# Optimization experiments

Measured on AMD Instinct MI355X. Metric: run time of the kernel, lower is better.

## Reference

```python
import jax, jax.numpy as jnp
import numpy as np

B, S, D, FF, H, N, P, K, KP, R = 2, 512, 256, 1024, 4, 512, 32, 16, 4, 64
DH = D // H  # 64


def _ln(x, g, b):
    mu = x.mean(-1, keepdims=True)
    var = ((x - mu) ** 2).mean(-1, keepdims=True)
    return (x - mu) * jax.lax.rsqrt(var + 1e-5) * g + b


def setup_inputs() -> dict:
    key = jax.random.key(0)
    ks = iter(jax.random.split(key, 40))
    nrm = lambda shape, std=0.02: jax.random.normal(next(ks), shape, jnp.float32) * std
    return dict(
        x=jax.random.normal(next(ks), (B, S, D), jnp.float32),
        g1=jnp.ones((D,), jnp.float32), b1=jnp.zeros((D,), jnp.float32),
        g2=jnp.ones((D,), jnp.float32), b2=jnp.zeros((D,), jnp.float32),
        Wq=nrm((D, D)), bq=jnp.zeros((D,), jnp.float32),
        Wk=nrm((D, D)), bk=jnp.zeros((D,), jnp.float32),
        Wv=nrm((D, D)), bv=jnp.zeros((D,), jnp.float32),
        Wpath=nrm((2 * D, 2)), bpath=jnp.zeros((2,), jnp.float32),
        neurons=nrm((N, D)),
        Wnq=nrm((D, D)), bnq=jnp.zeros((D,), jnp.float32),
        Wnk=nrm((D, D)), bnk=jnp.zeros((D,), jnp.float32),
        Wnv=nrm((D, D)), bnv=jnp.zeros((D,), jnp.float32),
        pattern_queries=nrm((P, D)),
        pattern_up_A=nrm((P, D, R)),
        pattern_up_B=nrm((P, R, FF), 0.01),
        Wub=nrm((D, FF), 0.01), bub=jnp.zeros((FF,), jnp.float32),
        Wd=nrm((FF, D), 0.02), bd=jnp.zeros((D,), jnp.float32),
    )


def _forward(x, g1, b1, g2, b2, Wq, bq, Wk, bk, Wv, bv, Wpath, bpath, neurons,
             Wnq, bnq, Wnk, bnk, Wnv, bnv, pattern_queries, pattern_up_A,
             pattern_up_B, Wub, bub, Wd, bd):
    # ---- NeuronRouter on norm1(x) ----
    n1 = _ln(x, g1, b1)
    q = (n1 @ Wq + bq).reshape(B, S, H, DH)
    k = (n1 @ Wk + bk).reshape(B, S, H, DH)
    v = (n1 @ Wv + bv).reshape(B, S, H, DH)
    attn = jax.nn.softmax(jnp.einsum('bqhd,bkhd->bhqk', q, k) / np.float32(np.sqrt(DH)), axis=-1)
    context = jnp.einsum('bhqk,bkhd->bqhd', attn, v).reshape(B, S, D)
    token_scores = n1 @ neurons.T        # [B,S,N]
    context_scores = context @ neurons.T
    w = jax.nn.softmax(jnp.concatenate([n1, context], -1) @ Wpath + bpath, axis=-1)
    scores = w[..., 0:1] * token_scores + w[..., 1:2] * context_scores
    topk_scores, topk_idx = jax.lax.top_k(scores, K)
    topk_w = jax.nn.softmax(topk_scores, axis=-1)      # [B,S,K]
    selected = neurons[topk_idx]                        # [B,S,K,D]

    # ---- InteractionFFN on norm2(x) ----
    n2 = _ln(x, g2, b2)
    qn = (selected @ Wnq + bnq).reshape(B, S, K, H, DH)
    kn = (selected @ Wnk + bnk).reshape(B, S, K, H, DH)
    vn = jax.nn.sigmoid((selected @ Wnv + bnv).reshape(B, S, K, H, DH))
    aw = jax.nn.softmax(jnp.einsum('bsqhd,bskhd->bshqk', qn, kn) / np.float32(np.sqrt(DH)), axis=-1)
    gates = jnp.einsum('bshqk,bskhd->bsqhd', aw, vn).reshape(B, S, K, D)
    aggregated = jnp.sum(topk_w[..., None] * (selected * gates), axis=2)  # [B,S,D]

    pattern_scores = 0.5 * (aggregated @ pattern_queries.T) / np.float32(np.sqrt(D)) \
                     + 0.5 * (context @ pattern_queries.T)               # [B,S,P]
    tps, tpi = jax.lax.top_k(pattern_scores, KP)
    tpw = jax.nn.softmax(tps, axis=-1)                                   # [B,S,KP]

    combined = n2 + aggregated
    A = pattern_up_A[tpi]    # [B,S,KP,D,R]  (gathered per-token LoRA A)
    Bm = pattern_up_B[tpi]   # [B,S,KP,R,FF] (gathered per-token LoRA B)
    h_mid = jnp.einsum('bsd,bskdr->bskr', combined, A)
    h_pat = jnp.einsum('bskr,bskrf->bskf', h_mid, Bm)
    h_pattern = jnp.sum(tpw[..., None] * h_pat, axis=2)                  # [B,S,FF]
    h = jax.nn.gelu(0.1 * (combined @ Wub + bub) + 0.9 * h_pattern, approximate=False)
    out = h @ Wd + bd
    return x + out, topk_idx


def reference(x, g1, b1, g2, b2, Wq, bq, Wk, bk, Wv, bv, Wpath, bpath, neurons,
              Wnq, bnq, Wnk, bnk, Wnv, bnv, pattern_queries, pattern_up_A,
              pattern_up_B, Wub, bub, Wd, bd):
    return _forward(x, g1, b1, g2, b2, Wq, bq, Wk, bk, Wv, bv, Wpath, bpath,
                    neurons, Wnq, bnq, Wnk, bnk, Wnv, bnv, pattern_queries,
                    pattern_up_A, pattern_up_B, Wub, bub, Wd, bd)
```

## Files before the change

kernel.cpp:

```cpp
#include <hip/hip_runtime.h>
#include <hip/hip_bf16.h>
#include <math.h>

#define BB 2
#define SS 512
#define DD 256
#define FFD 1024
#define HH 4
#define NN 512
#define PP 32
#define KK 16
#define KPP 4
#define RR 64
#define DHH 64
#define TT (BB*SS)
#define QT 16

__global__ __launch_bounds__(64) void zero_kernel(int* __restrict__ p, int n)
{
    int i = threadIdx.x;
    if (i < n) p[i] = 0;
}

__global__ __launch_bounds__(256) void ln_kernel(
    const float* __restrict__ x,
    const float* __restrict__ g1, const float* __restrict__ b1,
    const float* __restrict__ g2, const float* __restrict__ b2,
    float* __restrict__ n1, float* __restrict__ n2)
{
    int t = blockIdx.x;
    int d = threadIdx.x;
    __shared__ float red[256];
    float v = x[t*DD + d];
    red[d] = v; __syncthreads();
    for (int s = 128; s > 0; s >>= 1) { if (d < s) red[d] += red[d+s]; __syncthreads(); }
    float mu = red[0] * (1.0f/DD);
    __syncthreads();
    float dv = v - mu;
    red[d] = dv*dv; __syncthreads();
    for (int s = 128; s > 0; s >>= 1) { if (d < s) red[d] += red[d+s]; __syncthreads(); }
    float var = red[0] * (1.0f/DD);
    float r = 1.0f / sqrtf(var + 1e-5f);
    n1[t*DD+d] = dv*r*g1[d] + b1[d];
    n2[t*DD+d] = dv*r*g2[d] + b2[d];
}

__device__ __forceinline__ void gemm_body(
    const float* __restrict__ A, const float* __restrict__ Bm,
    const float* __restrict__ bias, const float* __restrict__ extra,
    float* __restrict__ C, int M, int Nn, int Kk, int transB, int mode,
    int k0off, int kLen)
{
    __shared__ float As[2][32][68];
    __shared__ float Bs[2][32][68];
    int bm = blockIdx.y * 64;
    int bn = blockIdx.x * 64;
    int tid = threadIdx.x;
    int tx = tid & 15, ty = tid >> 4;

    float4 pa[2], pb[2];

    #define LOAD_A(kbase) { \
        _Pragma("unroll") \
        for (int e = 0; e < 2; ++e) { \
            int r = e*32 + (tid>>3); int c4 = tid & 7; \
            pa[e] = *(const float4*)&A[(size_t)(bm + r)*Kk + (kbase) + c4*4]; \
        } }
    #define STORE_A(buf) { \
        _Pragma("unroll") \
        for (int e = 0; e < 2; ++e) { \
            int r = e*32 + (tid>>3); int c4 = tid & 7; \
            As[buf][c4*4+0][r] = pa[e].x; \
            As[buf][c4*4+1][r] = pa[e].y; \
            As[buf][c4*4+2][r] = pa[e].z; \
            As[buf][c4*4+3][r] = pa[e].w; \
        } }
    #define LOAD_B(kbase) { \
        if (transB == 0) { \
            _Pragma("unroll") \
            for (int e = 0; e < 2; ++e) { \
                int c = e*16 + (tid>>4); int n4 = tid & 15; \
                pb[e] = *(const float4*)&Bm[(size_t)((kbase) + c)*Nn + bn + n4*4]; \
            } \
        } else { \
            _Pragma("unroll") \
            for (int e = 0; e < 2; ++e) { \
                int r = e*32 + (tid>>3); int k4 = tid & 7; \
                pb[e] = *(const float4*)&Bm[(size_t)(bn + r)*Kk + (kbase) + k4*4]; \
            } \
        } }
    #define STORE_B(buf) { \
        if (transB == 0) { \
            _Pragma("unroll") \
            for (int e = 0; e < 2; ++e) { \
                int c = e*16 + (tid>>4); int n4 = tid & 15; \
                *(float4*)&Bs[buf][c][n4*4] = pb[e]; \
            } \
        } else { \
            _Pragma("unroll") \
            for (int e = 0; e < 2; ++e) { \
                int r = e*32 + (tid>>3); int k4 = tid & 7; \
                Bs[buf][k4*4+0][r] = pb[e].x; \
                Bs[buf][k4*4+1][r] = pb[e].y; \
                Bs[buf][k4*4+2][r] = pb[e].z; \
                Bs[buf][k4*4+3][r] = pb[e].w; \
            } \
        } }

    float acc[4][4] = {};
    int nk = kLen >> 5;

    LOAD_A(k0off); LOAD_B(k0off);
    STORE_A(0); STORE_B(0);
    __syncthreads();

    for (int kt = 0; kt < nk; ++kt) {
        int cur = kt & 1;
        if (kt + 1 < nk) { LOAD_A(k0off + (kt+1)*32); LOAD_B(k0off + (kt+1)*32); }
        #pragma unroll
        for (int kk = 0; kk < 32; ++kk) {
            float4 av = *(const float4*)&As[cur][kk][ty*4];
            float4 bv = *(const float4*)&Bs[cur][kk][tx*4];
            acc[0][0] = fmaf(av.x, bv.x, acc[0][0]);
            acc[0][1] = fmaf(av.x, bv.y, acc[0][1]);
            acc[0][2] = fmaf(av.x, bv.z, acc[0][2]);
            acc[0][3] = fmaf(av.x, bv.w, acc[0][3]);
            acc[1][0] = fmaf(av.y, bv.x, acc[1][0]);
            acc[1][1] = fmaf(av.y, bv.y, acc[1][1]);
            acc[1][2] = fmaf(av.y, bv.z, acc[1][2]);
            acc[1][3] = fmaf(av.y, bv.w, acc[1][3]);
            acc[2][0] = fmaf(av.z, bv.x, acc[2][0]);
            acc[2][1] = fmaf(av.z, bv.y, acc[2][1]);
            acc[2][2] = fmaf(av.z, bv.z, acc[2][2]);
            acc[2][3] = fmaf(av.z, bv.w, acc[2][3]);
            acc[3][0] = fmaf(av.w, bv.x, acc[3][0]);
            acc[3][1] = fmaf(av.w, bv.y, acc[3][1]);
            acc[3][2] = fmaf(av.w, bv.z, acc[3][2]);
            acc[3][3] = fmaf(av.w, bv.w, acc[3][3]);
        }
        if (kt + 1 < nk) {
            STORE_A(cur^1); STORE_B(cur^1);
            __syncthreads();
        }
    }

    #pragma unroll
    for (int i = 0; i < 4; ++i) {
        int m = bm + ty*4 + i;
        #pragma unroll
        for (int j = 0; j < 4; ++j) {
            int n = bn + tx*4 + j;
            float val = acc[i][j] + (bias ? bias[n] : 0.0f);
            if (mode == 1) {
                val = 1.0f / (1.0f + expf(-val));
            } else if (mode == 2) {
                size_t idx = (size_t)m*Nn + n;
                float hp = extra[idx] + extra[idx + (size_t)TT*FFD]
                         + extra[idx + 2*(size_t)TT*FFD] + extra[idx + 3*(size_t)TT*FFD];
                float z = 0.1f*val + 0.9f*hp;
                val = 0.5f*z*(1.0f + erff(z*0.70710678118654752f));
            } else if (mode == 3) {
                val = val + extra[(size_t)m*Nn+n];
            }
            C[(size_t)m*Nn + n] = val;
        }
    }
    #undef LOAD_A
    #undef STORE_A
    #undef LOAD_B
    #undef STORE_B
}

__global__ __launch_bounds__(256) void gemm_kernel(
    const float* __restrict__ A, const float* __restrict__ Bm,
    const float* __restrict__ bias, const float* __restrict__ extra,
    float* __restrict__ C, int M, int Nn, int Kk, int transB, int mode)
{
    gemm_body(A, Bm, bias, extra, C, M, Nn, Kk, transB, mode, 0, Kk);
}

struct GemmSet { const float* A; const float* B; const float* bias; float* C; int mode; };

__global__ __launch_bounds__(256) void gemm3_kernel(
    GemmSet s0, GemmSet s1, GemmSet s2, int M, int Nn, int Kk, int transB)
{
    GemmSet s = (blockIdx.z == 0) ? s0 : ((blockIdx.z == 1) ? s1 : s2);
    gemm_body(s.A, s.B, s.bias, nullptr, s.C, M, Nn, Kk, transB, s.mode, 0, Kk);
}

__global__ __launch_bounds__(256) void gemm_splitk_kernel(
    const float* __restrict__ A, const float* __restrict__ Bm,
    float* __restrict__ Cpart, int M, int Nn, int Kk, int kPerSplit)
{
    int sk = blockIdx.z;
    float* Cp = Cpart + (size_t)sk * M * Nn;
    gemm_body(A, Bm, nullptr, nullptr, Cp, M, Nn, Kk, 0, 0, sk*kPerSplit, kPerSplit);
}

__global__ __launch_bounds__(256) void combine_wd_kernel(
    const float* __restrict__ part, const float* __restrict__ x,
    const float* __restrict__ bd, float* __restrict__ out)
{
    int i = blockIdx.x*256 + threadIdx.x;
    int d = i & (DD-1);
    float s = x[i] + bd[d];
    s += part[i] + part[i + TT*DD] + part[i + 2*TT*DD] + part[i + 3*TT*DD];
    out[i] = s;
}

__global__ __launch_bounds__(256) void attn_kernel(
    const float* __restrict__ q, const float* __restrict__ k,
    const float* __restrict__ v, float* __restrict__ ctx)
{
    int bi = blockIdx.x;
    int qt = bi & 31;
    int bh = bi >> 5;
    int h = bh & (HH-1);
    int b = bh >> 2;
    int tid = threadIdx.x;
    int qo = tid >> 4;
    int c  = tid & 15;

    __shared__ float Qs[QT][68];
    __shared__ float Kt[64][64];
    __shared__ float Vs[64][68];
    __shared__ float Ps[QT][68];

    {
        const float* qp = q + ((size_t)(b*SS + qt*QT + qo)*DD) + h*DHH + c*4;
        *(float4*)&Qs[qo][c*4] = *(const float4*)qp;
    }
    float O0=0.f, O1=0.f, O2=0.f, O3=0.f;
    float mreg = -3.4e38f, lreg = 0.f;

    for (int t = 0; t < 8; ++t) {
        if (t) __syncthreads();
        #pragma unroll
        for (int e = 0; e < 4; ++e) {
            int lin = e*256 + tid;
            int kr = lin & 63;
            int c4 = lin >> 6;
            const float* kp = k + ((size_t)(b*SS + t*64 + kr)*DD) + h*DHH + c4*4;
            float4 kv = *(const float4*)kp;
            Kt[c4*4+0][kr] = kv.x;
            Kt[c4*4+1][kr] = kv.y;
            Kt[c4*4+2][kr] = kv.z;
            Kt[c4*4+3][kr] = kv.w;
            int vr = lin >> 4;
            int vc = lin & 15;
            const float* vp = v + ((size_t)(b*SS + t*64 + vr)*DD) + h*DHH + vc*4;
            *(float4*)&Vs[vr][vc*4] = *(const float4*)vp;
        }
        __syncthreads();
        float s0=0.f, s1=0.f, s2=0.f, s3=0.f;
        #pragma unroll 8
        for (int d = 0; d < 64; ++d) {
            float qv = Qs[qo][d];
            float4 kv = *(const float4*)&Kt[d][c*4];
            s0 = fmaf(qv, kv.x, s0);
            s1 = fmaf(qv, kv.y, s1);
            s2 = fmaf(qv, kv.z, s2);
            s3 = fmaf(qv, kv.w, s3);
        }
        s0 *= 0.125f; s1 *= 0.125f; s2 *= 0.125f; s3 *= 0.125f;
        float mx = fmaxf(fmaxf(s0, s1), fmaxf(s2, s3));
        #pragma unroll
        for (int mk = 1; mk <= 8; mk <<= 1)
            mx = fmaxf(mx, __shfl_xor(mx, mk));
        float mnew = fmaxf(mreg, mx);
        float scl = __expf(mreg - mnew);
        float e0 = __expf(s0 - mnew), e1 = __expf(s1 - mnew),
              e2 = __expf(s2 - mnew), e3 = __expf(s3 - mnew);
        float esum = e0 + e1 + e2 + e3;
        #pragma unroll
        for (int mk = 1; mk <= 8; mk <<= 1)
            esum += __shfl_xor(esum, mk);
        lreg = lreg * scl + esum;
        mreg = mnew;
        float4 pw; pw.x = e0; pw.y = e1; pw.z = e2; pw.w = e3;
        *(float4*)&Ps[qo][c*4] = pw;
        __syncthreads();
        O0 *= scl; O1 *= scl; O2 *= scl; O3 *= scl;
        #pragma unroll 8
        for (int kk = 0; kk < 64; ++kk) {
            float pv = Ps[qo][kk];
            float4 vv = *(const float4*)&Vs[kk][c*4];
            O0 = fmaf(pv, vv.x, O0);
            O1 = fmaf(pv, vv.y, O1);
            O2 = fmaf(pv, vv.z, O2);
            O3 = fmaf(pv, vv.w, O3);
        }
    }
    float linv = 1.0f / lreg;
    float4 o4; o4.x = O0*linv; o4.y = O1*linv; o4.z = O2*linv; o4.w = O3*linv;
    *(float4*)(ctx + ((size_t)(b*SS + qt*QT + qo)*DD) + h*DHH + c*4) = o4;
}

__global__ __launch_bounds__(256) void route_kernel(
    const float* __restrict__ n1, const float* __restrict__ ctx,
    const float* __restrict__ Wpath, const float* __restrict__ bpath,
    const float* __restrict__ ts, const float* __restrict__ cs,
    int* __restrict__ topk_idx, float* __restrict__ topk_w,
    float* __restrict__ out_idx)
{
    int t = blockIdx.x, tid = threadIdx.x;
    int wv = tid >> 6;
    __shared__ float pw0[4], pw1[4];
    float a = n1[t*DD+tid], c = ctx[t*DD+tid];
    float r0 = a * Wpath[tid*2+0] + c * Wpath[(DD+tid)*2+0];
    float r1 = a * Wpath[tid*2+1] + c * Wpath[(DD+tid)*2+1];
    #pragma unroll
    for (int off = 1; off < 64; off <<= 1) {
        r0 += __shfl_xor(r0, off);
        r1 += __shfl_xor(r1, off);
    }
    if ((tid & 63) == 0) { pw0[wv] = r0; pw1[wv] = r1; }
    __syncthreads();
    __shared__ float w0s, w1s;
    if (tid == 0) {
        float l0 = pw0[0]+pw0[1]+pw0[2]+pw0[3] + bpath[0];
        float l1 = pw1[0]+pw1[1]+pw1[2]+pw1[3] + bpath[1];
        float mm = fmaxf(l0, l1);
        float e0 = expf(l0-mm), e1 = expf(l1-mm);
        float is = 1.0f/(e0+e1);
        w0s = e0*is; w1s = e1*is;
    }
    __syncthreads();
    float w0 = w0s, w1 = w1s;
    __shared__ float sc[NN];
    sc[tid]     = w0*ts[t*NN+tid]     + w1*cs[t*NN+tid];
    sc[tid+256] = w0*ts[t*NN+tid+256] + w1*cs[t*NN+tid+256];
    __syncthreads();
    __shared__ float wvv[4]; __shared__ int wvi[4];
    __shared__ float selv[KK]; __shared__ int seli[KK];
    for (int it = 0; it < KK; ++it) {
        float v0 = sc[tid], v1 = sc[tid+256];
        float bv; int bi;
        if (v0 >= v1) { bv = v0; bi = tid; } else { bv = v1; bi = tid+256; }
        #pragma unroll
        for (int off = 1; off < 64; off <<= 1) {
            float ov = __shfl_xor(bv, off);
            int   oi = __shfl_xor(bi, off);
            if (ov > bv || (ov == bv && oi < bi)) { bv = ov; bi = oi; }
        }
        if ((tid & 63) == 0) { wvv[wv] = bv; wvi[wv] = bi; }
        __syncthreads();
        if (tid == 0) {
            float fv = wvv[0]; int fi = wvi[0];
            #pragma unroll
            for (int w = 1; w < 4; ++w) {
                float ov = wvv[w]; int oi = wvi[w];
                if (ov > fv || (ov == fv && oi < fi)) { fv = ov; fi = oi; }
            }
            selv[it] = fv; seli[it] = fi; sc[fi] = -3.4e38f;
        }
        __syncthreads();
    }
    if (tid == 0) {
        float mx = selv[0];
        float e[KK]; float sum = 0.f;
        for (int i = 0; i < KK; ++i) { e[i] = expf(selv[i]-mx); sum += e[i]; }
        float is = 1.0f/sum;
        for (int i = 0; i < KK; ++i) {
            topk_idx[t*KK+i] = seli[i];
            topk_w[t*KK+i]   = e[i]*is;
            out_idx[t*KK+i]  = (float)seli[i];
        }
    }
}

__global__ __launch_bounds__(256) void interact_kernel(
    const float* __restrict__ neurons,
    const float* __restrict__ nqa, const float* __restrict__ nka,
    const float* __restrict__ nva,
    const int* __restrict__ topk_idx, const float* __restrict__ topk_w,
    float* __restrict__ agg)
{
    int t = blockIdx.x, tid = threadIdx.x;
    __shared__ float nq[KK][DD+1];
    __shared__ float nk[KK][DD+1];
    __shared__ float nv[KK][DD+1];
    __shared__ float ps[HH][KK][KK];
    __shared__ float tw[KK];
    __shared__ int sidx[KK];
    if (tid < KK) { tw[tid] = topk_w[t*KK+tid]; sidx[tid] = topk_idx[t*KK+tid]; }
    __syncthreads();
    for (int i = 0; i < KK; ++i) {
        int idx = sidx[i];
        nq[i][tid] = nqa[idx*DD+tid];
        nk[i][tid] = nka[idx*DD+tid];
        nv[i][tid] = nva[idx*DD+tid];
    }
    __syncthreads();
    #pragma unroll
    for (int r = 0; r < 4; ++r) {
        int lin = r*256 + tid;
        int j = lin & 15, i = (lin >> 4) & 15, h = lin >> 8;
        const float* qp = &nq[i][h*DHH];
        const float* kp = &nk[j][h*DHH];
        float acc = 0.f;
        #pragma unroll 8
        for (int d = 0; d < DHH; ++d) acc = fmaf(qp[d], kp[d], acc);
        ps[h][i][j] = acc * 0.125f;
    }
    __syncthreads();
    if (tid < 64) {
        int h = tid >> 4, i = tid & 15;
        float mx = -3.4e38f;
        for (int j = 0; j < KK; ++j) mx = fmaxf(mx, ps[h][i][j]);
        float sum = 0.f;
        for (int j = 0; j < KK; ++j) { float e = expf(ps[h][i][j]-mx); ps[h][i][j] = e; sum += e; }
        float is = 1.0f/sum;
        for (int j = 0; j < KK; ++j) ps[h][i][j] *= is;
    }
    __syncthreads();
    int d = tid, h = d >> 6;
    float acc = 0.f;
    for (int i = 0; i < KK; ++i) {
        float g = 0.f;
        #pragma unroll
        for (int j = 0; j < KK; ++j) g = fmaf(ps[h][i][j], nv[j][d], g);
        acc += tw[i] * neurons[sidx[i]*DD + d] * g;
    }
    agg[t*DD+d] = acc;
}

__global__ __launch_bounds__(256) void pattern_select(
    const float* __restrict__ aggp, const float* __restrict__ ctxp,
    const float* __restrict__ n2p, const float* __restrict__ PQ,
    float* __restrict__ combined, float* __restrict__ tpwg,
    int* __restrict__ bin_count, int* __restrict__ bin_entry)
{
    int t = blockIdx.x, tid = threadIdx.x;
    __shared__ float mix[DD];
    __shared__ float ps[PP];
    __shared__ float psp[8][33];
    __shared__ int tpi[KPP];

    float a = aggp[t*DD+tid];
    float cx = ctxp[t*DD+tid];
    mix[tid] = 0.03125f * a + 0.5f * cx;
    combined[t*DD+tid] = n2p[t*DD+tid] + a;
    __syncthreads();

    {
        int p = tid & 31, g = tid >> 5;
        const float* pq = PQ + p*DD + g*32;
        const float* mp = mix + g*32;
        float acc = 0.f;
        #pragma unroll
        for (int d = 0; d < 32; ++d) acc = fmaf(mp[d], pq[d], acc);
        psp[g][p] = acc;
    }
    __syncthreads();
    if (tid < PP) {
        float s = 0.f;
        #pragma unroll
        for (int g = 0; g < 8; ++g) s += psp[g][tid];
        ps[tid] = s;
    }
    __syncthreads();

    if (tid == 0) {
        float vals[KPP];
        #pragma unroll
        for (int it = 0; it < KPP; ++it) {
            float bv = -3.4e38f; int bi = 0;
            for (int p = 0; p < PP; ++p) { float v = ps[p]; if (v > bv) { bv = v; bi = p; } }
            vals[it] = bv; tpi[it] = bi; ps[bi] = -3.4e38f;
        }
        float mx = vals[0];
        float e0 = expf(vals[0]-mx), e1 = expf(vals[1]-mx),
              e2 = expf(vals[2]-mx), e3 = expf(vals[3]-mx);
        float is = 1.0f/(e0+e1+e2+e3);
        tpwg[t*4+0]=e0*is; tpwg[t*4+1]=e1*is; tpwg[t*4+2]=e2*is; tpwg[t*4+3]=e3*is;
    }
    __syncthreads();
    if (tid < KPP) {
        int p = tpi[tid];
        int slot = atomicAdd(&bin_count[p], 1);
        bin_entry[p*TT + slot] = (t << 2) | tid;
    }
}

__global__ __launch_bounds__(256) void pattern_apply(
    const float* __restrict__ comb, const float* __restrict__ tpwg,
    const int* __restrict__ bin_count, const int* __restrict__ bin_entry,
    const float* __restrict__ Aup, const float* __restrict__ Bup,
    float* __restrict__ hpat4)
{
    int p = blockIdx.y, cch = blockIdx.x;
    int cnt = bin_count[p];
    int base = cch * 16;
    if (base >= cnt) return;
    int nt = cnt - base; if (nt > 16) nt = 16;
    int tid = threadIdx.x;

    __shared__ int toks[16]; __shared__ int kps[16]; __shared__ float wts[16];
    __shared__ float combs[16][DD+1];
    __shared__ float hmid[16][RR];

    if (tid < 16) {
        if (tid < nt) {
            int e = bin_entry[p*TT + base + tid];
            int t = e >> 2, kp = e & 3;
            toks[tid] = t; kps[tid] = kp; wts[tid] = tpwg[t*4 + kp];
        } else { toks[tid] = -1; wts[tid] = 0.f; }
    }
    __syncthreads();
    #pragma unroll
    for (int i = 0; i < 16; ++i) {
        int t = toks[i];
        combs[i][tid] = (t >= 0) ? comb[(size_t)t*DD + tid] : 0.f;
    }
    __syncthreads();

    {
        int i = tid >> 4, g = tid & 15;
        const float* Ap = Aup + (size_t)p*(DD*RR) + g*4;
        float a0=0.f, a1=0.f, a2=0.f, a3=0.f;
        #pragma unroll 8
        for (int d = 0; d < DD; ++d) {
            float cv = combs[i][d];
            float4 av = *(const float4*)&Ap[(size_t)d*RR];
            a0 = fmaf(cv, av.x, a0);
            a1 = fmaf(cv, av.y, a1);
            a2 = fmaf(cv, av.z, a2);
            a3 = fmaf(cv, av.w, a3);
        }
        float w = wts[i];
        hmid[i][g*4+0] = a0*w;
        hmid[i][g*4+1] = a1*w;
        hmid[i][g*4+2] = a2*w;
        hmid[i][g*4+3] = a3*w;
    }
    __syncthreads();

    float4 acc[16];
    #pragma unroll
    for (int i = 0; i < 16; ++i) acc[i] = make_float4(0.f,0.f,0.f,0.f);
    const float* Bp = Bup + (size_t)p*(RR*FFD) + tid*4;
    for (int r4 = 0; r4 < RR/4; ++r4) {
        float4 b0 = *(const float4*)&Bp[(size_t)(r4*4+0)*FFD];
        float4 b1 = *(const float4*)&Bp[(size_t)(r4*4+1)*FFD];
        float4 b2 = *(const float4*)&Bp[(size_t)(r4*4+2)*FFD];
        float4 b3 = *(const float4*)&Bp[(size_t)(r4*4+3)*FFD];
        #pragma unroll
        for (int i = 0; i < 16; ++i) {
            float4 h = *(const float4*)&hmid[i][r4*4];
            acc[i].x = fmaf(h.x,b0.x, fmaf(h.y,b1.x, fmaf(h.z,b2.x, fmaf(h.w,b3.x, acc[i].x))));
            acc[i].y = fmaf(h.x,b0.y, fmaf(h.y,b1.y, fmaf(h.z,b2.y, fmaf(h.w,b3.y, acc[i].y))));
            acc[i].z = fmaf(h.x,b0.z, fmaf(h.y,b1.z, fmaf(h.z,b2.z, fmaf(h.w,b3.z, acc[i].z))));
            acc[i].w = fmaf(h.x,b0.w, fmaf(h.y,b1.w, fmaf(h.z,b2.w, fmaf(h.w,b3.w, acc[i].w))));
        }
    }
    #pragma unroll
    for (int i = 0; i < 16; ++i) {
        int t = toks[i];
        if (t >= 0)
            *(float4*)&hpat4[(size_t)kps[i]*(TT*FFD) + (size_t)t*FFD + tid*4] = acc[i];
    }
}

extern "C" void kernel_launch(void* const* d_in, const int* in_sizes, int n_in,
                              void* d_out, int out_size, void* d_ws, size_t ws_size,
                              hipStream_t stream)
{
    const float* x        = (const float*)d_in[0];
    const float* g1       = (const float*)d_in[1];
    const float* b1       = (const float*)d_in[2];
    const float* g2       = (const float*)d_in[3];
    const float* b2       = (const float*)d_in[4];
    const float* Wq       = (const float*)d_in[5];
    const float* bq       = (const float*)d_in[6];
    const float* Wk       = (const float*)d_in[7];
    const float* bk       = (const float*)d_in[8];
    const float* Wv       = (const float*)d_in[9];
    const float* bv       = (const float*)d_in[10];
    const float* Wpath    = (const float*)d_in[11];
    const float* bpath    = (const float*)d_in[12];
    const float* neurons  = (const float*)d_in[13];
    const float* Wnq      = (const float*)d_in[14];
    const float* bnq      = (const float*)d_in[15];
    const float* Wnk      = (const float*)d_in[16];
    const float* bnk      = (const float*)d_in[17];
    const float* Wnv      = (const float*)d_in[18];
    const float* bnv      = (const float*)d_in[19];
    const float* PQ       = (const float*)d_in[20];
    const float* Aup      = (const float*)d_in[21];
    const float* Bup      = (const float*)d_in[22];
    const float* Wub      = (const float*)d_in[23];
    const float* bub      = (const float*)d_in[24];
    const float* Wd       = (const float*)d_in[25];
    const float* bd       = (const float*)d_in[26];

    float* out0    = (float*)d_out;
    float* out_idx = out0 + (size_t)TT*DD;

    float* ws = (float*)d_ws;
    float* n1    = ws; ws += TT*DD;
    float* n2    = ws; ws += TT*DD;
    float* qb    = ws; ws += TT*DD;
    float* kb    = ws; ws += TT*DD;
    float* vb    = ws; ws += TT*DD;
    float* ctx   = ws; ws += TT*DD;
    float* ts    = ws; ws += TT*NN;
    float* cs    = ws; ws += TT*NN;
    float* nqa   = ws; ws += NN*DD;
    float* nka   = ws; ws += NN*DD;
    float* nva   = ws; ws += NN*DD;
    float* agg   = ws; ws += TT*DD;
    float* comb  = ws; ws += TT*DD;
    float* hpat4 = ws; ws += 4*TT*FFD;
    float* hb    = ws; ws += TT*FFD;
    float* part  = ws; ws += 4*TT*DD;
    float* tkw   = ws; ws += TT*KK;
    float* tpwg  = ws; ws += TT*KPP;
    int*   tki   = (int*)ws; ws += TT*KK;
    int*   binc  = (int*)ws; ws += 32;
    int*   bine  = (int*)ws; ws += 32*TT;

    dim3 blk(256);

    zero_kernel<<<1, 64, 0, stream>>>(binc, 32);

    ln_kernel<<<TT, blk, 0, stream>>>(x, g1, b1, g2, b2, n1, n2);

    {
        GemmSet sq{n1, Wq, bq, qb, 0}, sk{n1, Wk, bk, kb, 0}, sv{n1, Wv, bv, vb, 0};
        gemm3_kernel<<<dim3(DD/64, TT/64, 3), blk, 0, stream>>>(sq, sk, sv, TT, DD, DD, 0);
    }

    {
        GemmSet s0{neurons, Wnq, bnq, nqa, 0}, s1{neurons, Wnk, bnk, nka, 0},
                s2{neurons, Wnv, bnv, nva, 1};
        gemm3_kernel<<<dim3(DD/64, NN/64, 3), blk, 0, stream>>>(s0, s1, s2, NN, DD, DD, 0);
    }

    attn_kernel<<<BB*HH*(SS/QT), blk, 0, stream>>>(qb, kb, vb, ctx);

    {
        GemmSet s0{n1, neurons, nullptr, ts, 0}, s1{ctx, neurons, nullptr, cs, 0};
        gemm3_kernel<<<dim3(NN/64, TT/64, 2), blk, 0, stream>>>(s0, s1, s1, TT, NN, DD, 1);
    }

    route_kernel<<<TT, blk, 0, stream>>>(n1, ctx, Wpath, bpath, ts, cs, tki, tkw, out_idx);

    interact_kernel<<<TT, blk, 0, stream>>>(neurons, nqa, nka, nva, tki, tkw, agg);

    pattern_select<<<TT, blk, 0, stream>>>(agg, ctx, n2, PQ, comb, tpwg, binc, bine);

    pattern_apply<<<dim3(TT/16, PP), blk, 0, stream>>>(comb, tpwg, binc, bine, Aup, Bup, hpat4);

    gemm_kernel<<<dim3(FFD/64, TT/64), blk, 0, stream>>>(comb, Wub, bub, hpat4, hb, TT, FFD, DD, 0, 2);

    gemm_splitk_kernel<<<dim3(DD/64, TT/64, 4), blk, 0, stream>>>(hb, Wd, part, TT, DD, FFD, FFD/4);
    combine_wd_kernel<<<TT*DD/256, blk, 0, stream>>>(part, x, bd, out0);
}
```

Baseline: 342.3 us.

## Split pattern LoRA into two kernels staging A and B tiles in LDS

The fused per-16-token pattern_apply kernel is split into two kernels. lora_mid loads each pattern's A matrix (64 KB) into shared memory once and loops over that pattern's bin entries, writing the weighted mid activations to a new global buffer. lora_apply tiles the FF dimension into 128-wide slices, keeps the B slice in LDS and processes entries in chunks of 64. The goal is to stop re-reading A and B from global memory for every 16-token chunk. The cost is an extra launch, a round trip through global memory for the mid activations, and a large LDS footprint that lowers occupancy, while load imbalance across uneven bins may serialise some blocks.

```diff
diff --git a/kernel.cpp b/kernel.cpp
--- a/kernel.cpp
+++ b/kernel.cpp
@@ -483,82 +483,122 @@
     }
 }
 
-__global__ __launch_bounds__(256) void pattern_apply(
+__global__ __launch_bounds__(256) void lora_mid(
     const float* __restrict__ comb, const float* __restrict__ tpwg,
     const int* __restrict__ bin_count, const int* __restrict__ bin_entry,
-    const float* __restrict__ Aup, const float* __restrict__ Bup,
-    float* __restrict__ hpat4)
-{
-    int p = blockIdx.y, cch = blockIdx.x;
+    const float* __restrict__ Aup, float* __restrict__ hmid_g)
+{
+    int p = blockIdx.x, sub = blockIdx.y;
     int cnt = bin_count[p];
-    int base = cch * 16;
-    if (base >= cnt) return;
-    int nt = cnt - base; if (nt > 16) nt = 16;
+    if (sub * 16 >= cnt) return;
     int tid = threadIdx.x;
 
-    __shared__ int toks[16]; __shared__ int kps[16]; __shared__ float wts[16];
-    __shared__ float combs[16][DD+1];
-    __shared__ float hmid[16][RR];
-
-    if (tid < 16) {
-        if (tid < nt) {
-            int e = bin_entry[p*TT + base + tid];
-            int t = e >> 2, kp = e & 3;
-            toks[tid] = t; kps[tid] = kp; wts[tid] = tpwg[t*4 + kp];
-        } else { toks[tid] = -1; wts[tid] = 0.f; }
-    }
-    __syncthreads();
+    __shared__ float As[DD][RR];
+    __shared__ float combs[16][DD+4];
+    __shared__ int es[16];
+
+    const float* Ap = Aup + (size_t)p*(DD*RR);
     #pragma unroll
-    for (int i = 0; i < 16; ++i) {
-        int t = toks[i];
-        combs[i][tid] = (t >= 0) ? comb[(size_t)t*DD + tid] : 0.f;
-    }
-    __syncthreads();
-
-    {
-        int i = tid >> 4, g = tid & 15;
-        const float* Ap = Aup + (size_t)p*(DD*RR) + g*4;
+    for (int e = 0; e < 64; ++e) {
+        int lin = e*256 + tid;
+        int d = lin >> 4, rg = lin & 15;
+        *(float4*)&As[d][rg*4] = *(const float4*)&Ap[(size_t)d*RR + rg*4];
+    }
+
+    for (int base = sub*16; base < cnt; base += 8*16) {
+        int nt = cnt - base; if (nt > 16) nt = 16;
+        __syncthreads();
+        if (tid < 16) es[tid] = (tid < nt) ? bin_entry[p*TT + base + tid] : -1;
+        __syncthreads();
+        #pragma unroll
+        for (int i = 0; i < 16; ++i) {
+            int e = es[i];
+            combs[i][tid] = (e >= 0) ? comb[(size_t)(e >> 2)*DD + tid] : 0.f;
+        }
+        __syncthreads();
+
+        int i = tid >> 4, rg = tid & 15;
         float a0=0.f, a1=0.f, a2=0.f, a3=0.f;
         #pragma unroll 8
         for (int d = 0; d < DD; ++d) {
             float cv = combs[i][d];
-            float4 av = *(const float4*)&Ap[(size_t)d*RR];
+            float4 av = *(const float4*)&As[d][rg*4];
             a0 = fmaf(cv, av.x, a0);
             a1 = fmaf(cv, av.y, a1);
             a2 = fmaf(cv, av.z, a2);
             a3 = fmaf(cv, av.w, a3);
         }
-        float w = wts[i];
-        hmid[i][g*4+0] = a0*w;
-        hmid[i][g*4+1] = a1*w;
-        hmid[i][g*4+2] = a2*w;
-        hmid[i][g*4+3] = a3*w;
-    }
-    __syncthreads();
-
-    float4 acc[16];
+        int e = es[i];
+        if (e >= 0) {
+            float w = tpwg[e];
+            float4 o; o.x = a0*w; o.y = a1*w; o.z = a2*w; o.w = a3*w;
+            *(float4*)&hmid_g[(size_t)e*RR + rg*4] = o;
+        }
+    }
+}
+
+__global__ __launch_bounds__(256) void lora_apply(
+    const int* __restrict__ bin_count, const int* __restrict__ bin_entry,
+    const float* __restrict__ hmid_g, const float* __restrict__ Bup,
+    float* __restrict__ hpat4)
+{
+    int p = blockIdx.x, ff0 = blockIdx.y * 128;
+    int cnt = bin_count[p];
+    int tid = threadIdx.x;
+
+    __shared__ float Bs[RR][132];
+    __shared__ float hm[64][68];
+    __shared__ int es[64];
+
+    const float* Bp = Bup + (size_t)p*(RR*FFD) + ff0;
     #pragma unroll
-    for (int i = 0; i < 16; ++i) acc[i] = make_float4(0.f,0.f,0.f,0.f);
-    const float* Bp = Bup + (size_t)p*(RR*FFD) + tid*4;
-    for (int r4 = 0; r4 < RR/4; ++r4) {
-        float4 b0 = *(const float4*)&Bp[(size_t)(r4*4+0)*FFD];
-        float4 b1 = *(const float4*)&Bp[(size_t)(r4*4+1)*FFD];
-        float4 b2 = *(const float4*)&Bp[(size_t)(r4*4+2)*FFD];
-        float4 b3 = *(const float4*)&Bp[(size_t)(r4*4+3)*FFD];
-        #pragma unroll
-        for (int i = 0; i < 16; ++i) {
-            float4 h = *(const float4*)&hmid[i][r4*4];
-            acc[i].x = fmaf(h.x,b0.x, fmaf(h.y,b1.x, fmaf(h.z,b2.x, fmaf(h.w,b3.x, acc[i].x))));
-            acc[i].y = fmaf(h.x,b0.y, fmaf(h.y,b1.y, fmaf(h.z,b2.y, fmaf(h.w,b3.y, acc[i].y))));
-            acc[i].z = fmaf(h.x,b0.z, fmaf(h.y,b1.z, fmaf(h.z,b2.z, fmaf(h.w,b3.z, acc[i].z))));
-            acc[i].w = fmaf(h.x,b0.w, fmaf(h.y,b1.w, fmaf(h.z,b2.w, fmaf(h.w,b3.w, acc[i].w))));
-        }
-    }
-    #pragma unroll
-    for (int i = 0; i < 16; ++i) {
-        int t = toks[i];
-        if (t >= 0)
-            *(float4*)&hpat4[(size_t)kps[i]*(TT*FFD) + (size_t)t*FFD + tid*4] = acc[i];
+    for (int e = 0; e < 8; ++e) {
+        int lin = e*256 + tid;
+        int r = lin >> 5, cg = lin & 31;
+        *(float4*)&Bs[r][cg*4] = *(const float4*)&Bp[(size_t)r*FFD + cg*4];
+    }
+
+    int eg = tid >> 5, cg = tid & 31;
+
+    for (int base = 0; base < cnt; base += 64) {
+        int nt = cnt - base; if (nt > 64) nt = 64;
+        __syncthreads();
+        if (tid < 64) es[tid] = (tid < nt) ? bin_entry[p*TT + base + tid] : -1;
+        __syncthreads();
+        #pragma unroll
+        for (int e = 0; e < 4; ++e) {
+            int lin = e*256 + tid;
+            int i = lin >> 4, rg = lin & 15;
+            int ei = es[i];
+            float4 hv = make_float4(0.f,0.f,0.f,0.f);
+            if (ei >= 0) hv = *(const float4*)&hmid_g[(size_t)ei*RR + rg*4];
+            *(float4*)&hm[i][rg*4] = hv;
+        }
+        __syncthreads();
+
+        float4 acc[8];
+        #pragma unroll
+        for (int j = 0; j < 8; ++j) acc[j] = make_float4(0.f,0.f,0.f,0.f);
+        #pragma unroll 4
+        for (int r = 0; r < RR; ++r) {
+            float4 b = *(const float4*)&Bs[r][cg*4];
+            #pragma unroll
+            for (int j = 0; j < 8; ++j) {
+                float h = hm[eg*8+j][r];
+                acc[j].x = fmaf(h, b.x, acc[j].x);
+                acc[j].y = fmaf(h, b.y, acc[j].y);
+                acc[j].z = fmaf(h, b.z, acc[j].z);
+                acc[j].w = fmaf(h, b.w, acc[j].w);
+            }
+        }
+        #pragma unroll
+        for (int j = 0; j < 8; ++j) {
+            int e = es[eg*8+j];
+            if (e >= 0) {
+                int t = e >> 2, kp = e & 3;
+                *(float4*)&hpat4[(size_t)kp*(TT*FFD) + (size_t)t*FFD + ff0 + cg*4] = acc[j];
+            }
+        }
     }
 }
 
@@ -614,6 +654,7 @@
     float* hpat4 = ws; ws += 4*TT*FFD;
     float* hb    = ws; ws += TT*FFD;
     float* part  = ws; ws += 4*TT*DD;
+    float* hmidg = ws; ws += 4*TT*RR;
     float* tkw   = ws; ws += TT*KK;
     float* tpwg  = ws; ws += TT*KPP;
     int*   tki   = (int*)ws; ws += TT*KK;
@@ -650,7 +691,9 @@
 
     pattern_select<<<TT, blk, 0, stream>>>(agg, ctx, n2, PQ, comb, tpwg, binc, bine);
 
-    pattern_apply<<<dim3(TT/16, PP), blk, 0, stream>>>(comb, tpwg, binc, bine, Aup, Bup, hpat4);
+    lora_mid<<<dim3(PP, 8), blk, 0, stream>>>(comb, tpwg, binc, bine, Aup, hmidg);
+
+    lora_apply<<<dim3(PP, FFD/128), blk, 0, stream>>>(binc, bine, hmidg, Bup, hpat4);
 
     gemm_kernel<<<dim3(FFD/64, TT/64), blk, 0, stream>>>(comb, Wub, bub, hpat4, hb, TT, FFD, DD, 0, 2);
 
```

Result: slower. 414.2 us (+21.0%).
